# Performance work log

Measured on AMD Instinct MI355X. Metric: run time of the kernel, lower is better.

The kernel has to match this reference:

```python
import jax, jax.numpy as jnp
from jax import lax
import numpy as np

STRIDE = 2
EXT_PAD = (2, 2)  # computed in __init__: (total_pad - inter_pad)//2 split symmetrically


def setup_inputs() -> dict:
    key = jax.random.key(0)
    k1, k2, k3 = jax.random.split(key, 3)
    x = jax.random.normal(k1, (32, 256, 32, 32), dtype=jnp.float32)
    # Conv kernel in OIHW layout: [out_chs, in_chs, kh, kw]
    W = jax.random.normal(k2, (128, 256, 4, 4), dtype=jnp.float32) * 0.05
    b = jax.random.normal(k3, (128,), dtype=jnp.float32) * 0.01
    return {"x": x, "W": W, "b": b}


def reference(x, W, b):
    # _Interpad: insert (stride-1) zeros between every pair of adjacent spatial
    # elements (not after the last one): new_size = (size-1)*stride + 1.
    B, C, H, Wd = x.shape
    s = STRIDE
    stuffed = jnp.zeros((B, C, (H - 1) * s + 1, (Wd - 1) * s + 1), dtype=x.dtype)
    stuffed = stuffed.at[:, :, ::s, ::s].set(x)
    # external zero padding
    p = EXT_PAD
    padded = jnp.pad(stuffed, ((0, 0), (0, 0), p, p))
    # standard (cross-correlation) conv, stride 1, dilation 1, valid padding
    y = lax.conv_general_dilated(
        padded, W,
        window_strides=(1, 1),
        padding='VALID',
        rhs_dilation=(1, 1),
        dimension_numbers=('NCHW', 'OIHW', 'NCHW'),
    )
    return y + b[None, :, None, None]
```

## Files before the change

kernel.cpp:

```cpp
#include <hip/hip_runtime.h>


typedef float  f32x4  __attribute__((ext_vector_type(4)));
typedef short  short8 __attribute__((ext_vector_type(8)));
typedef unsigned short ushort4v __attribute__((ext_vector_type(4)));
typedef unsigned short ushort8v __attribute__((ext_vector_type(8)));

__device__ __forceinline__ unsigned short f2bf(float f) {
    unsigned u = __builtin_bit_cast(unsigned, f);
    u += 0x7fffu + ((u >> 16) & 1u);
    return (unsigned short)(u >> 16);
}

__device__ __forceinline__ void ld_lds16(const unsigned short* g, unsigned short* l) {
    __builtin_amdgcn_global_load_lds(
        (const __attribute__((address_space(1))) unsigned int*)g,
        (__attribute__((address_space(3))) unsigned int*)l,
        16, 0, 0);
}

#define XP_U 288
#define XP_G 9792
#define XP_N 313344
#define WP_G 8192
#define WP_PI 262144
#define WROW 1040
#define WBUFS 8320

__global__ __launch_bounds__(256) void prepack_w2(const float* __restrict__ W,
                                                  unsigned short* __restrict__ wp) {
    int t = blockIdx.x * 256 + threadIdx.x;
    int o = t >> 8, c = t & 255;
    int g = c >> 3, c8 = c & 7;
    const float4* src = (const float4*)(W + (size_t)(o * 256 + c) * 16);
    float4 q0 = src[0], q1 = src[1], q2 = src[2], q3 = src[3];
    float rows[4][4] = {{q0.x,q0.y,q0.z,q0.w},{q1.x,q1.y,q1.z,q1.w},
                        {q2.x,q2.y,q2.z,q2.w},{q3.x,q3.y,q3.z,q3.w}};
    #pragma unroll
    for (int pi = 0; pi < 2; ++pi)
    #pragma unroll
    for (int pj = 0; pj < 2; ++pj)
    #pragma unroll
    for (int du = 0; du < 2; ++du)
    #pragma unroll
    for (int dv = 0; dv < 2; ++dv)
        wp[pi*WP_PI + g*WP_G + pj*4096 + (du*2+dv)*1024 + o*8 + c8] =
            f2bf(rows[pi+2*du][pj+2*dv]);
}

__global__ __launch_bounds__(256) void prepack_x(const float* __restrict__ x,
                                                 unsigned short* __restrict__ xp) {
    __shared__ unsigned short xt[256 * 32];
    const int tid = threadIdx.x;
    const int up  = blockIdx.x;
    const int n   = blockIdx.y;
    const bool interior = (up >= 1 && up <= 32);

    if (interior) {
        const int u = up - 1;
        #pragma unroll
        for (int k = 0; k < 8; ++k) {
            int idx4 = tid + k * 256;
            int c = idx4 >> 3, v4 = idx4 & 7;
            float4 val = *(const float4*)(x + ((size_t)(n*256 + c)*32 + u)*32 + v4*4);
            ushort4v s = { f2bf(val.x), f2bf(val.y), f2bf(val.z), f2bf(val.w) };
            *(ushort4v*)&xt[c*32 + v4*4] = s;
        }
        __syncthreads();
    }

    #pragma unroll
    for (int s = 0; s < 5; ++s) {
        int id = tid + s * 256;
        if (id < 1152) {
            int g = id / 36, vp = id % 36;
            ushort8v o8 = {0,0,0,0,0,0,0,0};
            if (interior && vp >= 1 && vp <= 32) {
                #pragma unroll
                for (int e = 0; e < 8; ++e)
                    o8[e] = xt[(g*8 + e)*32 + (vp - 1)];
            }
            *(ushort8v*)&xp[(size_t)n*XP_N + g*XP_G + up*XP_U + vp*8] = o8;
        }
    }
}

__global__ __launch_bounds__(256, 2) void tconv_main(
    const unsigned short* __restrict__ xp,
    const unsigned short* __restrict__ wp,
    const float* __restrict__ bias,
    float* __restrict__ out)
{
    __shared__ __align__(16) unsigned short lds[33280];
    unsigned short* wsh0 = lds;

    const int tid  = threadIdx.x;
    const int lane = tid & 63;
    const int w    = tid >> 6;
    const int pjw  = w >> 1;
    const int half = w & 1;
    const int lg   = lane >> 4;
    const int ln   = lane & 15;
    const int du   = lg >> 1, dv = lg & 1;

    const int bid = blockIdx.x;
    const int wg  = (bid & 7) * 64 + (bid >> 3);
    const int n   = wg >> 4;
    const int aq  = (wg >> 1) & 7;
    const int pi  = wg & 1;
    const int a0  = aq * 4;

    const unsigned short* xpb = xp + (size_t)n * XP_N + (a0 + pi) * XP_U;
    const unsigned short* wpb = wp + pi * WP_PI;

    int xoff[4];
    #pragma unroll
    for (int jj = 0; jj < 4; ++jj) {
        int rr = half * 2 + (jj >> 1) + du;
        int vv = (jj & 1) * 16 + ln + pjw + dv;
        xoff[jj] = rr * XP_U + vv * 8;
    }
    const int wfoff = (pjw * 4 + lg) * WROW + ln * 8;

    f32x4 acc[8][4];
    #pragma unroll
    for (int i = 0; i < 8; ++i)
        #pragma unroll
        for (int jj = 0; jj < 4; ++jj)
            acc[i][jj] = (f32x4){0.f, 0.f, 0.f, 0.f};

    short8 xA[4], xB[4];

#define STAGE_W(CH, WBUF)                                                    \
    { const unsigned short* ws_ = wpb + (size_t)(CH) * WP_G;                 \
      unsigned short* wd_ = wsh0 + (WBUF) * WBUFS;                           \
      _Pragma("unroll")                                                      \
      for (int s_ = 0; s_ < 4; ++s_) {                                       \
          int r_ = w * 2 + (s_ >> 1), h_ = s_ & 1;                           \
          ld_lds16(ws_ + r_ * 1024 + h_ * 512 + lane * 8,                    \
                   wd_ + r_ * WROW + h_ * 512); } }

#define LOAD_X(CH, XS)                                                      \
    { const unsigned short* xs_ = xpb + (size_t)(CH) * XP_G;                 \
      _Pragma("unroll")                                                      \
      for (int jj_ = 0; jj_ < 4; ++jj_)                                      \
          XS[jj_] = *(const short8*)(xs_ + xoff[jj_]); }

#define CHUNK(BUF, XS, CH, VMN, DO_W, DO_X)                                  \
    {                                                                        \
        __builtin_amdgcn_sched_barrier(0);                                   \
        asm volatile("s_waitcnt vmcnt(" #VMN ")" ::: "memory");              \
        __builtin_amdgcn_s_barrier();                                        \
        __builtin_amdgcn_sched_barrier(0);                                   \
        if (DO_W) STAGE_W((CH) + 3, ((BUF) + 3) & 3);                        \
        const unsigned short* wb_ = wsh0 + (BUF) * WBUFS + wfoff;            \
        _Pragma("unroll")                                                    \
        for (int i_ = 0; i_ < 8; ++i_) {                                     \
            short8 av_ = *(const short8*)&wb_[i_ * 128];                     \
            _Pragma("unroll")                                                \
            for (int jj_ = 0; jj_ < 4; ++jj_)                                \
                acc[i_][jj_] = __builtin_amdgcn_mfma_f32_16x16x32_bf16(      \
                    av_, XS[jj_], acc[i_][jj_], 0, 0, 0);                    \
        }                                                                    \
        if (DO_X) LOAD_X((CH) + 2, XS);                                      \
    }

    STAGE_W(0, 0);
    STAGE_W(1, 1);
    __builtin_amdgcn_sched_barrier(0);
    LOAD_X(0, xA);
    __builtin_amdgcn_sched_barrier(0);
    STAGE_W(2, 2);
    __builtin_amdgcn_sched_barrier(0);
    LOAD_X(1, xB);
    __builtin_amdgcn_sched_barrier(0);

    for (int ch4 = 0; ch4 < 28; ch4 += 4) {
        CHUNK(0, xA, ch4 + 0, 8, 1, 1);
        CHUNK(1, xB, ch4 + 1, 8, 1, 1);
        CHUNK(2, xA, ch4 + 2, 8, 1, 1);
        CHUNK(3, xB, ch4 + 3, 8, 1, 1);
    }
    CHUNK(0, xA, 28, 8, 1, 1);
    CHUNK(1, xB, 29, 8, 0, 1);
    CHUNK(2, xA, 30, 4, 0, 0);
    CHUNK(3, xB, 31, 0, 0, 0);

#undef CHUNK
#undef LOAD_X
#undef STAGE_W

    float* epi = (float*)lds;
    #pragma unroll
    for (int i = 0; i < 8; ++i) {
        __syncthreads();
        f32x4 bv = *(const f32x4*)&bias[i * 16 + lg * 4];
        #pragma unroll
        for (int jj = 0; jj < 4; ++jj) {
            int ar = half * 2 + (jj >> 1);
            int b  = (jj & 1) * 16 + ln;
            #pragma unroll
            for (int r = 0; r < 4; ++r)
                epi[((lg * 4 + r) * 8 + ar * 2 + pjw) * 33 + b] = acc[i][jj][r] + bv[r];
        }
        __syncthreads();
        #pragma unroll
        for (int k = 0; k < 4; ++k) {
            int f   = tid + k * 256;
            int row = f >> 4;
            int q   = f & 15;
            float4 v;
            v.x = epi[(row * 2 + 0) * 33 + q * 2 + 0];
            v.y = epi[(row * 2 + 1) * 33 + q * 2 + 0];
            v.z = epi[(row * 2 + 0) * 33 + q * 2 + 1];
            v.w = epi[(row * 2 + 1) * 33 + q * 2 + 1];
            int o     = i * 16 + (row >> 2);
            int i_out = 2 * (a0 + (row & 3)) + pi;
            *(float4*)&out[(((size_t)n * 128 + o) * 64 + i_out) * 64 + q * 4] = v;
        }
    }
}

__global__ __launch_bounds__(256) void prepack_w(const float* __restrict__ W,
                                                 unsigned short* __restrict__ Wp) {
    int t = blockIdx.x * 256 + threadIdx.x;
    int o = t >> 8, c = t & 255;
    const float4* src = (const float4*)(W + (size_t)(o * 256 + c) * 16);
    float4 q0 = src[0], q1 = src[1], q2 = src[2], q3 = src[3];
    float rows[4][4] = {{q0.x,q0.y,q0.z,q0.w},{q1.x,q1.y,q1.z,q1.w},
                        {q2.x,q2.y,q2.z,q2.w},{q3.x,q3.y,q3.z,q3.w}};
    #pragma unroll
    for (int pi = 0; pi < 2; ++pi)
    #pragma unroll
    for (int pj = 0; pj < 2; ++pj)
    #pragma unroll
    for (int du = 0; du < 2; ++du)
    #pragma unroll
    for (int dv = 0; dv < 2; ++dv)
        Wp[((((pi*2+pj)*4 + du*2+dv)*128 + o)*256) + c] = f2bf(rows[pi+2*du][pj+2*dv]);
}

template<bool PRE>
__global__ __launch_bounds__(512, 2) void tconv_mfma(
    const float* __restrict__ x, const float* __restrict__ W,
    const unsigned short* __restrict__ Wp, const float* __restrict__ bias,
    float* __restrict__ out)
{
    __shared__ __align__(16) unsigned short xsh[2][9 * 34 * 8];
    __shared__ __align__(16) unsigned short wsh[2][2 * 4 * 128 * 8];

    const int tid = threadIdx.x;
    const int bid = blockIdx.x;
    const int pi  = bid & 1;
    const int aq  = (bid >> 1) & 3;
    const int n   = bid >> 3;
    const int a0  = aq * 8;
    const int u0  = a0 + pi - 1;

    const int l   = tid & 63;
    const int w   = tid >> 6;
    const int pjw = w >> 2;
    const int q   = w & 3;
    const int lg  = l >> 4;
    const int ln  = l & 15;

    const int sv = tid & 31;
    const int sg = tid >> 5;

    f32x4 acc[8][4];
    #pragma unroll
    for (int i = 0; i < 8; ++i)
        #pragma unroll
        for (int jj = 0; jj < 4; ++jj)
            acc[i][jj] = (f32x4){0.f, 0.f, 0.f, 0.f};

    float    xv[5];
    ushort4v wv[4];
    float4   wa[2], wb[2];

    auto stage_load = [&](int ch) {
        const int c0 = ch * 8;
        #pragma unroll
        for (int s = 0; s < 5; ++s) {
            int p = sg * 5 + s;
            if (p < 72) {
                int c = p & 7, rr = p >> 3;
                int u = u0 + rr;
                xv[s] = ((unsigned)u < 32u)
                      ? x[((n*256 + c0 + c)*32 + u)*32 + sv] : 0.f;
            }
        }
        if (PRE) {
            #pragma unroll
            for (int k = 0; k < 4; ++k) {
                int uu = tid + k * 512;
                int chalf = uu & 1, o = (uu >> 1) & 127;
                int sub = (uu >> 8) & 3, pjq = (uu >> 10) & 1;
                wv[k] = *(const ushort4v*)&Wp[(((pi*2 + pjq)*4 + sub)*128 + o)*256
                                              + c0 + chalf*4];
            }
        } else {
            #pragma unroll
            for (int k = 0; k < 2; ++k) {
                int pr = tid + k * 512;
                int o = pr >> 3, c = pr & 7;
                const float* base = W + ((o*256 + c0 + c) << 4) + pi*4;
                wa[k] = *(const float4*)base;
                wb[k] = *(const float4*)(base + 8);
            }
        }
    };

    auto stage_write = [&](int buf) {
        #pragma unroll
        for (int s = 0; s < 5; ++s) {
            int p = sg * 5 + s;
            if (p < 72) {
                int c = p & 7, rr = p >> 3;
                xsh[buf][(rr*34 + sv + 1)*8 + c] = f2bf(xv[s]);
            }
        }
        if (tid < 144) {
            int pr = tid >> 1;
            int rr = pr >> 3, c = pr & 7;
            int cw = (tid & 1) * 33;
            xsh[buf][(rr*34 + cw)*8 + c] = 0;
        }
        if (PRE) {
            #pragma unroll
            for (int k = 0; k < 4; ++k) {
                int uu = tid + k * 512;
                int chalf = uu & 1, o = (uu >> 1) & 127;
                int sub = (uu >> 8) & 3, pjq = (uu >> 10) & 1;
                *(ushort4v*)&wsh[buf][(((pjq*4 + sub)*128 + o)*8) + chalf*4] = wv[k];
            }
        } else {
            #pragma unroll
            for (int k = 0; k < 2; ++k) {
                int pr = tid + k * 512;
                int o = pr >> 3, c = pr & 7;
                float ra[4] = {wa[k].x, wa[k].y, wa[k].z, wa[k].w};
                float rb[4] = {wb[k].x, wb[k].y, wb[k].z, wb[k].w};
                #pragma unroll
                for (int pj2 = 0; pj2 < 2; ++pj2)
                #pragma unroll
                for (int duu = 0; duu < 2; ++duu)
                #pragma unroll
                for (int dvv = 0; dvv < 2; ++dvv) {
                    float val = duu ? rb[pj2 + 2*dvv] : ra[pj2 + 2*dvv];
                    wsh[buf][(((pj2*4 + duu*2 + dvv)*128 + o)*8) + c] = f2bf(val);
                }
            }
        }
    };

    stage_load(0);
    stage_write(0);
    __syncthreads();

    for (int ch = 0; ch < 32; ++ch) {
        const int cur = ch & 1;
        if (ch + 1 < 32) stage_load(ch + 1);

        short8 bfr[4];
        #pragma unroll
        for (int jj = 0; jj < 4; ++jj) {
            int arow = q*2 + (jj >> 1);
            int b    = (jj & 1)*16 + ln;
            int rr   = arow + (lg >> 1);
            int cw   = b + pjw + (lg & 1);
            bfr[jj]  = *(const short8*)&xsh[cur][(rr*34 + cw)*8];
        }
        #pragma unroll
        for (int i = 0; i < 8; ++i) {
            short8 av = *(const short8*)&wsh[cur][((pjw*4 + lg)*128 + i*16 + ln)*8];
            #pragma unroll
            for (int jj = 0; jj < 4; ++jj)
                acc[i][jj] = __builtin_amdgcn_mfma_f32_16x16x32_bf16(
                                 av, bfr[jj], acc[i][jj], 0, 0, 0);
        }

        if (ch + 1 < 32) stage_write(cur ^ 1);
        __syncthreads();
    }

    #pragma unroll
    for (int i = 0; i < 8; ++i) {
        const f32x4 bv = *(const f32x4*)&bias[i*16 + lg*4];
        #pragma unroll
        for (int jj = 0; jj < 4; ++jj) {
            int arow  = q*2 + (jj >> 1);
            int b     = (jj & 1)*16 + ln;
            int i_out = 2*(a0 + arow) + pi;
            int j_out = 2*b + pjw;
            int o0    = i*16 + lg*4;
            int base  = ((n*128 + o0)*64 + i_out)*64 + j_out;
            #pragma unroll
            for (int r = 0; r < 4; ++r)
                out[base + r*4096] = acc[i][jj][r] + bv[r];
        }
    }
}

extern "C" void kernel_launch(void* const* d_in, const int* in_sizes, int n_in,
                              void* d_out, int out_size, void* d_ws, size_t ws_size,
                              hipStream_t stream) {
    const float* x    = (const float*)d_in[0];
    const float* W    = (const float*)d_in[1];
    const float* bias = (const float*)d_in[2];
    float* out        = (float*)d_out;

    const size_t wp2_bytes = (size_t)2 * WP_PI * 2;
    const size_t xp_bytes  = (size_t)32 * XP_N * 2;
    if (ws_size >= wp2_bytes + xp_bytes) {
        unsigned short* wp2 = (unsigned short*)d_ws;
        unsigned short* xpp = (unsigned short*)((char*)d_ws + wp2_bytes);
        prepack_w2<<<128, 256, 0, stream>>>(W, wp2);
        prepack_x<<<dim3(34, 32), 256, 0, stream>>>(x, xpp);
        tconv_main<<<512, 256, 0, stream>>>(xpp, wp2, bias, out);
    } else if (ws_size >= (size_t)4*4*128*256*2) {
        unsigned short* Wp = (unsigned short*)d_ws;
        prepack_w<<<128, 256, 0, stream>>>(W, Wp);
        tconv_mfma<true><<<256, 512, 0, stream>>>(x, W, Wp, bias, out);
    } else {
        tconv_mfma<false><<<256, 512, 0, stream>>>(x, W, nullptr, bias, out);
    }
}
```

Before: 55.32 us.

## Merge prepack kernels, drop LDS padding, add MFMA priority and vectorised epilogue

Folds the weight and input prepack kernels into one launch, with the extra grid columns handling the weights, so one kernel launch is saved. It shrinks the weight LDS row pitch from 1040 to 1024 and gives global_load_lds an explicit per-lane destination offset, and wraps the MFMA block in s_setprio so the compute wave gets priority. The epilogue row order is permuted so reads become float2 pairs, and a barrier is added before LDS is reused. Removing the padding may bring back LDS bank conflicts on the fragment reads.

```diff
diff --git a/kernel.cpp b/kernel.cpp
--- a/kernel.cpp
+++ b/kernel.cpp
@@ -24,36 +24,39 @@
 #define XP_N 313344
 #define WP_G 8192
 #define WP_PI 262144
-#define WROW 1040
-#define WBUFS 8320
-
-__global__ __launch_bounds__(256) void prepack_w2(const float* __restrict__ W,
-                                                  unsigned short* __restrict__ wp) {
-    int t = blockIdx.x * 256 + threadIdx.x;
-    int o = t >> 8, c = t & 255;
-    int g = c >> 3, c8 = c & 7;
-    const float4* src = (const float4*)(W + (size_t)(o * 256 + c) * 16);
-    float4 q0 = src[0], q1 = src[1], q2 = src[2], q3 = src[3];
-    float rows[4][4] = {{q0.x,q0.y,q0.z,q0.w},{q1.x,q1.y,q1.z,q1.w},
-                        {q2.x,q2.y,q2.z,q2.w},{q3.x,q3.y,q3.z,q3.w}};
-    #pragma unroll
-    for (int pi = 0; pi < 2; ++pi)
-    #pragma unroll
-    for (int pj = 0; pj < 2; ++pj)
-    #pragma unroll
-    for (int du = 0; du < 2; ++du)
-    #pragma unroll
-    for (int dv = 0; dv < 2; ++dv)
-        wp[pi*WP_PI + g*WP_G + pj*4096 + (du*2+dv)*1024 + o*8 + c8] =
-            f2bf(rows[pi+2*du][pj+2*dv]);
-}
-
-__global__ __launch_bounds__(256) void prepack_x(const float* __restrict__ x,
-                                                 unsigned short* __restrict__ xp) {
+#define WROW 1024
+#define WBUFS 8192
+
+__global__ __launch_bounds__(256) void prepack_all(
+    const float* __restrict__ x, const float* __restrict__ W,
+    unsigned short* __restrict__ wp, unsigned short* __restrict__ xpp)
+{
+    const int tid = threadIdx.x;
+    if (blockIdx.x >= 34) {
+        int wid = (blockIdx.x - 34) * 32 + blockIdx.y;
+        int t = wid * 256 + tid;
+        int o = t >> 8, c = t & 255;
+        int g = c >> 3, c8 = c & 7;
+        const float4* src = (const float4*)(W + (size_t)(o * 256 + c) * 16);
+        float4 q0 = src[0], q1 = src[1], q2 = src[2], q3 = src[3];
+        float rows[4][4] = {{q0.x,q0.y,q0.z,q0.w},{q1.x,q1.y,q1.z,q1.w},
+                            {q2.x,q2.y,q2.z,q2.w},{q3.x,q3.y,q3.z,q3.w}};
+        #pragma unroll
+        for (int pi = 0; pi < 2; ++pi)
+        #pragma unroll
+        for (int pj = 0; pj < 2; ++pj)
+        #pragma unroll
+        for (int du = 0; du < 2; ++du)
+        #pragma unroll
+        for (int dv = 0; dv < 2; ++dv)
+            wp[pi*WP_PI + g*WP_G + pj*4096 + (du*2+dv)*1024 + o*8 + c8] =
+                f2bf(rows[pi+2*du][pj+2*dv]);
+        return;
+    }
+
     __shared__ unsigned short xt[256 * 32];
-    const int tid = threadIdx.x;
-    const int up  = blockIdx.x;
-    const int n   = blockIdx.y;
+    const int up = blockIdx.x;
+    const int n  = blockIdx.y;
     const bool interior = (up >= 1 && up <= 32);
 
     if (interior) {
@@ -80,7 +83,7 @@
                 for (int e = 0; e < 8; ++e)
                     o8[e] = xt[(g*8 + e)*32 + (vp - 1)];
             }
-            *(ushort8v*)&xp[(size_t)n*XP_N + g*XP_G + up*XP_U + vp*8] = o8;
+            *(ushort8v*)&xpp[(size_t)n*XP_N + g*XP_G + up*XP_U + vp*8] = o8;
         }
     }
 }
@@ -91,7 +94,7 @@
     const float* __restrict__ bias,
     float* __restrict__ out)
 {
-    __shared__ __align__(16) unsigned short lds[33280];
+    __shared__ __align__(16) unsigned short lds[32768];
     unsigned short* wsh0 = lds;
 
     const int tid  = threadIdx.x;
@@ -138,7 +141,7 @@
       for (int s_ = 0; s_ < 4; ++s_) {                                       \
           int r_ = w * 2 + (s_ >> 1), h_ = s_ & 1;                           \
           ld_lds16(ws_ + r_ * 1024 + h_ * 512 + lane * 8,                    \
-                   wd_ + r_ * WROW + h_ * 512); } }
+                   wd_ + r_ * WROW + h_ * 512 + lane * 8); } }
 
 #define LOAD_X(CH, XS)                                                      \
     { const unsigned short* xs_ = xpb + (size_t)(CH) * XP_G;                 \
@@ -154,6 +157,7 @@
         __builtin_amdgcn_sched_barrier(0);                                   \
         if (DO_W) STAGE_W((CH) + 3, ((BUF) + 3) & 3);                        \
         const unsigned short* wb_ = wsh0 + (BUF) * WBUFS + wfoff;            \
+        __builtin_amdgcn_s_setprio(1);                                       \
         _Pragma("unroll")                                                    \
         for (int i_ = 0; i_ < 8; ++i_) {                                     \
             short8 av_ = *(const short8*)&wb_[i_ * 128];                     \
@@ -162,6 +166,7 @@
                 acc[i_][jj_] = __builtin_amdgcn_mfma_f32_16x16x32_bf16(      \
                     av_, XS[jj_], acc[i_][jj_], 0, 0, 0);                    \
         }                                                                    \
+        __builtin_amdgcn_s_setprio(0);                                       \
         if (DO_X) LOAD_X((CH) + 2, XS);                                      \
     }
 
@@ -190,6 +195,8 @@
 #undef LOAD_X
 #undef STAGE_W
 
+    __syncthreads();
+
     float* epi = (float*)lds;
     #pragma unroll
     for (int i = 0; i < 8; ++i) {
@@ -201,20 +208,19 @@
             int b  = (jj & 1) * 16 + ln;
             #pragma unroll
             for (int r = 0; r < 4; ++r)
-                epi[((lg * 4 + r) * 8 + ar * 2 + pjw) * 33 + b] = acc[i][jj][r] + bv[r];
+                epi[((r * 4 + lg) * 8 + ar * 2 + pjw) * 33 + b] = acc[i][jj][r] + bv[r];
         }
         __syncthreads();
         #pragma unroll
         for (int k = 0; k < 4; ++k) {
-            int f   = tid + k * 256;
-            int row = f >> 4;
-            int q   = f & 15;
-            float4 v;
-            v.x = epi[(row * 2 + 0) * 33 + q * 2 + 0];
-            v.y = epi[(row * 2 + 1) * 33 + q * 2 + 0];
-            v.z = epi[(row * 2 + 0) * 33 + q * 2 + 1];
-            v.w = epi[(row * 2 + 1) * 33 + q * 2 + 1];
-            int o     = i * 16 + (row >> 2);
+            int f    = tid + k * 256;
+            int row  = f >> 4;
+            int q    = f & 15;
+            float2 A = *(const float2*)&epi[(row * 2 + 0) * 33 + q * 2];
+            float2 B = *(const float2*)&epi[(row * 2 + 1) * 33 + q * 2];
+            float4 v = { A.x, B.x, A.y, B.y };
+            int olp   = row >> 2;
+            int o     = i * 16 + ((olp & 3) << 2) + (olp >> 2);
             int i_out = 2 * (a0 + (row & 3)) + pi;
             *(float4*)&out[(((size_t)n * 128 + o) * 64 + i_out) * 64 + q * 4] = v;
         }
@@ -415,8 +421,7 @@
     if (ws_size >= wp2_bytes + xp_bytes) {
         unsigned short* wp2 = (unsigned short*)d_ws;
         unsigned short* xpp = (unsigned short*)((char*)d_ws + wp2_bytes);
-        prepack_w2<<<128, 256, 0, stream>>>(W, wp2);
-        prepack_x<<<dim3(34, 32), 256, 0, stream>>>(x, xpp);
+        prepack_all<<<dim3(38, 32), 256, 0, stream>>>(x, W, wp2, xpp);
         tconv_main<<<512, 256, 0, stream>>>(xpp, wp2, bias, out);
     } else if (ws_size >= (size_t)4*4*128*256*2) {
         unsigned short* Wp = (unsigned short*)d_ws;
```

Measured after the change: 55.89 us. Within noise of the previous version (+1.0%).
